# Optimization experiments

Hardware: AMD Instinct MI355X
Metric: run time of the kernel (lower is better)

Reference implementation:

```python
import jax, jax.numpy as jnp
from jax import lax
import numpy as np

B, CIN, COUT, T, H, W, KH, KW = 8, 256, 256, 16, 28, 28, 3, 3


def setup_inputs() -> dict:
    key = jax.random.key(0)
    k1, k2, k3 = jax.random.split(key, 3)
    x = jax.random.normal(k1, (B, CIN, T, H, W), dtype=jnp.float32)
    alpha = jax.random.uniform(k2, (B, CIN, T, 1, 1), dtype=jnp.float32)
    # base weight, kaiming-uniform-like init, stored as [1,1,c_out,c_in,kh,kw]
    fan_in = CIN * KH * KW
    bound = 1.0 / np.sqrt(fan_in)
    weight = jax.random.uniform(k3, (1, 1, COUT, CIN, KH, KW), dtype=jnp.float32,
                                minval=-bound, maxval=bound)
    return {"x": x, "alpha": alpha, "weight": weight}


def reference(x, alpha, weight):
    # x: [b, c_in, t, h, w]; alpha: [b, c_in, t, 1, 1]; weight: [1,1,c_out,c_in,kh,kw]
    b, c_in, t, h, w = x.shape
    c_out = weight.shape[2]
    w_base = weight[0, 0]  # [c_out, c_in, kh, kw]
    # W_t = alpha_t * W_base scales only input channels (alpha broadcasts over c_out),
    # so (alpha*W) conv x == W conv (alpha*x): modulate input, then one shared conv.
    xm = x * alpha  # [b, c_in, t, h, w]
    xm = jnp.transpose(xm, (0, 2, 1, 3, 4)).reshape(b * t, c_in, h, w)
    y = lax.conv_general_dilated(
        xm, w_base,
        window_strides=(1, 1),
        padding=((1, 1), (1, 1)),
        dimension_numbers=("NCHW", "OIHW", "NCHW"),
    )  # [b*t, c_out, h, w]
    oh, ow = y.shape[-2], y.shape[-1]
    y = y.reshape(b, t, c_out, oh, ow)
    return jnp.transpose(y, (0, 2, 1, 3, 4))  # [b, c_out, t, h, w]
```

## Files before the change

kernel.cpp:

```cpp
#include <hip/hip_runtime.h>
#include <hip/hip_bf16.h>
#include <cstdint>

#define CIN   256
#define COUT  256
#define NB    8
#define NT    16
#define NH    28
#define NW    28
#define HP    30
#define WP    30

#define XM_ELEMS   ((size_t)NB * NT * HP * WP * CIN)
#define XM_BYTES   (XM_ELEMS * 2)

typedef __bf16 bf16x8 __attribute__((ext_vector_type(8)));
typedef float  f32x4  __attribute__((ext_vector_type(4)));

#define AS1 __attribute__((address_space(1)))
#define AS3 __attribute__((address_space(3)))

static __device__ __forceinline__ unsigned short f2bf(float f) {
    __hip_bfloat16 h = __float2bfloat16(f);
    return __builtin_bit_cast(unsigned short, h);
}

__global__ void modulate_kernel(const float* __restrict__ x,
                                const float* __restrict__ alpha,
                                unsigned short* __restrict__ xm) {
    const int ci = threadIdx.x;
    const int blk = blockIdx.x;
    const int hp = blk % 30;
    const int bt = blk / 30;
    unsigned short* row = xm + (size_t)(bt * 900 + hp * 30) * 256;
    if (hp == 0 || hp == 29) {
        #pragma unroll
        for (int wp = 0; wp < 30; ++wp) row[wp * 256 + ci] = 0;
        return;
    }
    const int t = bt & 15, b = bt >> 4;
    const int h = hp - 1;
    const float a = alpha[(b * CIN + ci) * NT + t];
    const float* xrow = x + ((size_t)((b * CIN + ci) * NT + t) * NH + h) * NW;
    row[ci] = 0;
    row[29 * 256 + ci] = 0;
    const float4* xv = (const float4*)xrow;
    #pragma unroll
    for (int q = 0; q < 7; ++q) {
        float4 v = xv[q];
        row[(q * 4 + 1) * 256 + ci] = f2bf(v.x * a);
        row[(q * 4 + 2) * 256 + ci] = f2bf(v.y * a);
        row[(q * 4 + 3) * 256 + ci] = f2bf(v.z * a);
        row[(q * 4 + 4) * 256 + ci] = f2bf(v.w * a);
    }
}

__global__ void repack_w_kernel(const float* __restrict__ w,
                                unsigned short* __restrict__ wB) {
    const int ci = threadIdx.x;
    const int tap = blockIdx.x >> 8;
    const int co  = blockIdx.x & 255;
    wB[((tap * 256 + co) * 256) + ci] = f2bf(w[(co * 256 + ci) * 9 + tap]);
}


#define BAR()    __builtin_amdgcn_s_barrier()
#define LGKM0()  asm volatile("s_waitcnt lgkmcnt(0)" ::: "memory")
#define VMW(N)   asm volatile("s_waitcnt vmcnt(" #N ")" ::: "memory")
#define SCHED0() __builtin_amdgcn_sched_barrier(0)
#define PRIO(x)  __builtin_amdgcn_s_setprio(x)

#define STAGE_F(P) do {                                                       \
    const int kh2 = (tap2 * 11) >> 5;                                         \
    const int kw2 = tap2 - 3 * kh2;                                           \
    const int aOff = tap2 * 65536 + cic2 * 32;                                \
    const int bOff = ((kh2 - 1) * 30 + (kw2 - 1)) * 256 + cic2 * 32;          \
    _Pragma("unroll") for (int c_ = 0; c_ < 2; ++c_)                          \
        __builtin_amdgcn_global_load_lds(                                     \
            (const AS1 void*)(aSrc + aOff + c_ * 32768),                      \
            (AS3 void*)(lds + (P)*32768 + (c_*128 + wave*16)*64 + lane*16),   \
            16, 0, 0);                                                        \
    _Pragma("unroll") for (int c_ = 0; c_ < 2; ++c_)                          \
        __builtin_amdgcn_global_load_lds(                                     \
            (const AS1 void*)(bL[c_] + bOff),                                 \
            (AS3 void*)(lds + (P)*32768 + 16384 + (c_*128 + wave*16)*64 + lane*16), \
            16, 0, 0);                                                        \
    if (++tap2 == 9) { tap2 = 0; ++cic2; }                                    \
} while (0)

#define READF(S, P) do {                                                      \
    _Pragma("unroll") for (int m_ = 0; m_ < 4; ++m_)                          \
        fa##S[m_] = *(const bf16x8*)(lds + (P)*32768 +                        \
            (wm*64 + m_*16 + l15)*64 + readSwz);                              \
    _Pragma("unroll") for (int f_ = 0; f_ < 7; ++f_)                          \
        fb##S[f_] = *(const bf16x8*)(lds + (P)*32768 + 16384 +                \
            (wn*112 + f_*16 + l15)*64 + readSwz);                             \
} while (0)

#define MFMA28(S) do {                                                        \
    _Pragma("unroll") for (int m_ = 0; m_ < 4; ++m_)                          \
    _Pragma("unroll") for (int f_ = 0; f_ < 7; ++f_)                          \
        acc[m_][f_] = __builtin_amdgcn_mfma_f32_16x16x32_bf16(                \
            fb##S[f_], fa##S[m_], acc[m_][f_], 0, 0, 0);                      \
} while (0)

#define BODY_S(CS, NS, NBUF, SBUF) do {                                       \
    VMW(4);                                                                   \
    SCHED0();                                                                 \
    BAR();                                                                    \
    READF(NS, NBUF);                                                          \
    STAGE_F(SBUF);                                                            \
    SCHED0();                                                                 \
    PRIO(1); MFMA28(CS); PRIO(0);                                             \
    LGKM0();                                                                  \
    SCHED0();                                                                 \
} while (0)

#define BODY_N(CS, NS, NBUF, VMN) do {                                        \
    VMW(VMN);                                                                 \
    SCHED0();                                                                 \
    BAR();                                                                    \
    READF(NS, NBUF);                                                          \
    SCHED0();                                                                 \
    PRIO(1); MFMA28(CS); PRIO(0);                                             \
    LGKM0();                                                                  \
    SCHED0();                                                                 \
} while (0)

__global__ __launch_bounds__(512, 2) void conv_gemm_kernel(
    const unsigned short* __restrict__ xm,
    const unsigned short* __restrict__ wB,
    float* __restrict__ out) {
    __shared__ __align__(1024) char lds[98304];

    const int tid  = threadIdx.x;
    const int wave = tid >> 6;
    const int lane = tid & 63;
    const int l15  = lane & 15;
    const int n0   = blockIdx.x * 224;
    const int wm   = wave >> 1;
    const int wn   = wave & 1;

    const int swzE = 8 * ((lane & 3) ^ ((lane >> 3) & 3));
    const unsigned short* aSrc = wB + (wave * 16 + (lane >> 2)) * 256 + swzE;

    const unsigned short* bL[2];
    #pragma unroll
    for (int c_ = 0; c_ < 2; ++c_) {
        int nl = c_ * 128 + wave * 16 + (lane >> 2);
        nl = nl > 223 ? 223 : nl;
        const int n  = n0 + nl;
        const int w_ = n % 28, h_ = (n / 28) % 28, bt = n / 784;
        bL[c_] = xm + (size_t)((bt * 30 + h_ + 1) * 30 + (w_ + 1)) * 256 + swzE;
    }

    const int readSwz = ((lane >> 4) ^ ((l15 >> 1) & 3)) << 4;

    f32x4 acc[4][7];
    #pragma unroll
    for (int i = 0; i < 4; ++i)
        #pragma unroll
        for (int j = 0; j < 7; ++j) acc[i][j] = f32x4{0.f, 0.f, 0.f, 0.f};

    bf16x8 faA[4], fbA[7], faB[4], fbB[7];

    int tap2 = 0, cic2 = 0;
    STAGE_F(0);
    STAGE_F(1);
    STAGE_F(2);
    VMW(8);
    SCHED0();
    BAR();
    READF(A, 0);
    LGKM0();
    SCHED0();

    #pragma unroll 1
    for (int it = 0; it < 11; ++it) {
        BODY_S(A, B, 1, 0);
        BODY_S(B, A, 2, 1);
        BODY_S(A, B, 0, 2);
        BODY_S(B, A, 1, 0);
        BODY_S(A, B, 2, 1);
        BODY_S(B, A, 0, 2);
    }
    BODY_S(A, B, 1, 0);
    BODY_S(B, A, 2, 1);
    BODY_S(A, B, 0, 2);
    BODY_N(B, A, 1, 4);
    BODY_N(A, B, 2, 0);
    PRIO(1); MFMA28(B); PRIO(0);

    #pragma unroll
    for (int f = 0; f < 7; ++f) {
        const int n  = n0 + wn * 112 + f * 16 + ((lane >> 4) << 2);
        const int bt = n / 784;
        const int hw = n - bt * 784;
        const int b = bt >> 4, t = bt & 15;
        float* obase = out + ((size_t)(b * 256) * 16 + t) * 784 + hw;
        #pragma unroll
        for (int m = 0; m < 4; ++m) {
            const int co = wm * 64 + m * 16 + l15;
            *(f32x4*)(obase + (size_t)co * 12544) = acc[m][f];
        }
    }
}

extern "C" void kernel_launch(void* const* d_in, const int* in_sizes, int n_in,
                              void* d_out, int out_size, void* d_ws, size_t ws_size,
                              hipStream_t stream) {
    const float* x      = (const float*)d_in[0];
    const float* alpha  = (const float*)d_in[1];
    const float* weight = (const float*)d_in[2];
    float* out = (float*)d_out;

    unsigned short* xm = (unsigned short*)d_ws;
    unsigned short* wB = (unsigned short*)((char*)d_ws + XM_BYTES);

    modulate_kernel<<<dim3(NB * NT * HP), dim3(256), 0, stream>>>(x, alpha, xm);
    repack_w_kernel<<<dim3(9 * 256), dim3(256), 0, stream>>>(weight, wB);
    conv_gemm_kernel<<<dim3(448), dim3(512), 0, stream>>>(xm, wB, out);
}
```

Measured before the change: 158.3 us.

## Load weight fragments directly from global into registers, halve LDS staging

The weight (A) operand is no longer staged through LDS with global_load_lds. Each wave now reads its own weight fragments straight from global memory into registers, one step ahead of use. Only the activation tiles stay in the triple-buffered LDS ring, which halves the shared-memory footprint and could let two blocks share a CU. The cost is redundant global/L2 traffic for weights across waves, and the wait counts are retuned to cover the added in-flight loads, so exposed latency is a risk.

```diff
diff --git a/kernel.cpp b/kernel.cpp
--- a/kernel.cpp
+++ b/kernel.cpp
@@ -70,30 +70,28 @@
 #define SCHED0() __builtin_amdgcn_sched_barrier(0)
 #define PRIO(x)  __builtin_amdgcn_s_setprio(x)
 
-#define STAGE_F(P) do {                                                       \
-    const int kh2 = (tap2 * 11) >> 5;                                         \
-    const int kw2 = tap2 - 3 * kh2;                                           \
-    const int aOff = tap2 * 65536 + cic2 * 32;                                \
-    const int bOff = ((kh2 - 1) * 30 + (kw2 - 1)) * 256 + cic2 * 32;          \
-    _Pragma("unroll") for (int c_ = 0; c_ < 2; ++c_)                          \
-        __builtin_amdgcn_global_load_lds(                                     \
-            (const AS1 void*)(aSrc + aOff + c_ * 32768),                      \
-            (AS3 void*)(lds + (P)*32768 + (c_*128 + wave*16)*64 + lane*16),   \
-            16, 0, 0);                                                        \
+#define STAGE_B(P) do {                                                       \
+    const int kh2 = (tapS * 11) >> 5;                                         \
+    const int kw2 = tapS - 3 * kh2;                                           \
+    const int bOff = ((kh2 - 1) * 30 + (kw2 - 1)) * 256 + cicS * 32;          \
     _Pragma("unroll") for (int c_ = 0; c_ < 2; ++c_)                          \
         __builtin_amdgcn_global_load_lds(                                     \
             (const AS1 void*)(bL[c_] + bOff),                                 \
-            (AS3 void*)(lds + (P)*32768 + 16384 + (c_*128 + wave*16)*64 + lane*16), \
+            (AS3 void*)(lds + (P)*16384 + (c_*128 + wave*16)*64 + lane*16),   \
             16, 0, 0);                                                        \
-    if (++tap2 == 9) { tap2 = 0; ++cic2; }                                    \
-} while (0)
-
-#define READF(S, P) do {                                                      \
+    if (++tapS == 9) { tapS = 0; ++cicS; }                                    \
+} while (0)
+
+#define LOADA(S) do {                                                         \
+    const unsigned short* ap_ = aRow + tapA * 65536 + cicA * 32;              \
     _Pragma("unroll") for (int m_ = 0; m_ < 4; ++m_)                          \
-        fa##S[m_] = *(const bf16x8*)(lds + (P)*32768 +                        \
-            (wm*64 + m_*16 + l15)*64 + readSwz);                              \
+        fa##S[m_] = *(const bf16x8*)(ap_ + m_ * 4096);                        \
+    if (++tapA == 9) { tapA = 0; ++cicA; }                                    \
+} while (0)
+
+#define READF_B(S, P) do {                                                    \
     _Pragma("unroll") for (int f_ = 0; f_ < 7; ++f_)                          \
-        fb##S[f_] = *(const bf16x8*)(lds + (P)*32768 + 16384 +                \
+        fb##S[f_] = *(const bf16x8*)(lds + (P)*16384 +                        \
             (wn*112 + f_*16 + l15)*64 + readSwz);                             \
 } while (0)
 
@@ -105,11 +103,12 @@
 } while (0)
 
 #define BODY_S(CS, NS, NBUF, SBUF) do {                                       \
-    VMW(4);                                                                   \
+    VMW(6);                                                                   \
     SCHED0();                                                                 \
     BAR();                                                                    \
-    READF(NS, NBUF);                                                          \
-    STAGE_F(SBUF);                                                            \
+    READF_B(NS, NBUF);                                                        \
+    LOADA(NS);                                                                \
+    STAGE_B(SBUF);                                                            \
     SCHED0();                                                                 \
     PRIO(1); MFMA28(CS); PRIO(0);                                             \
     LGKM0();                                                                  \
@@ -120,7 +119,8 @@
     VMW(VMN);                                                                 \
     SCHED0();                                                                 \
     BAR();                                                                    \
-    READF(NS, NBUF);                                                          \
+    READF_B(NS, NBUF);                                                        \
+    LOADA(NS);                                                                \
     SCHED0();                                                                 \
     PRIO(1); MFMA28(CS); PRIO(0);                                             \
     LGKM0();                                                                  \
@@ -131,7 +131,7 @@
     const unsigned short* __restrict__ xm,
     const unsigned short* __restrict__ wB,
     float* __restrict__ out) {
-    __shared__ __align__(1024) char lds[98304];
+    __shared__ __align__(1024) char lds[49152];
 
     const int tid  = threadIdx.x;
     const int wave = tid >> 6;
@@ -141,9 +141,10 @@
     const int wm   = wave >> 1;
     const int wn   = wave & 1;
 
+    const unsigned short* aRow =
+        wB + (wm * 64 + l15) * 256 + (lane >> 4) * 8;
+
     const int swzE = 8 * ((lane & 3) ^ ((lane >> 3) & 3));
-    const unsigned short* aSrc = wB + (wave * 16 + (lane >> 2)) * 256 + swzE;
-
     const unsigned short* bL[2];
     #pragma unroll
     for (int c_ = 0; c_ < 2; ++c_) {
@@ -164,14 +165,17 @@
 
     bf16x8 faA[4], fbA[7], faB[4], fbB[7];
 
-    int tap2 = 0, cic2 = 0;
-    STAGE_F(0);
-    STAGE_F(1);
-    STAGE_F(2);
+    int tapS = 0, cicS = 0;
+    int tapA = 0, cicA = 0;
+
+    STAGE_B(0);
+    STAGE_B(1);
+    LOADA(A);
+    STAGE_B(2);
     VMW(8);
     SCHED0();
     BAR();
-    READF(A, 0);
+    READF_B(A, 0);
     LGKM0();
     SCHED0();
 
@@ -187,8 +191,8 @@
     BODY_S(A, B, 1, 0);
     BODY_S(B, A, 2, 1);
     BODY_S(A, B, 0, 2);
-    BODY_N(B, A, 1, 4);
-    BODY_N(A, B, 2, 0);
+    BODY_N(B, A, 1, 6);
+    BODY_N(A, B, 2, 4);
     PRIO(1); MFMA28(B); PRIO(0);
 
     #pragma unroll
```

Result: slower. 244.2 us (+54.2%).

## Shrink conv GEMM block tile to 256x112 with four waves

Applied to the files above, without the earlier changes.

The GEMM tile changes from 256 output channels by 224 pixels with 8 waves to 256 by 112 with 4 waves. Each wave now owns a full 64-channel slice across the whole 112-pixel column. The grid doubles to 896 blocks, and LDS per block drops to 72KB across three stages. The aim is better load balance across CUs and more resident blocks, at the cost of weight tiles being reloaded twice as often, which lowers arithmetic intensity per block.

```diff
diff --git a/kernel.cpp b/kernel.cpp
--- a/kernel.cpp
+++ b/kernel.cpp
@@ -71,30 +71,30 @@
 #define PRIO(x)  __builtin_amdgcn_s_setprio(x)
 
 #define STAGE_F(P) do {                                                       \
-    const int kh2 = (tap2 * 11) >> 5;                                         \
-    const int kw2 = tap2 - 3 * kh2;                                           \
-    const int aOff = tap2 * 65536 + cic2 * 32;                                \
-    const int bOff = ((kh2 - 1) * 30 + (kw2 - 1)) * 256 + cic2 * 32;          \
-    _Pragma("unroll") for (int c_ = 0; c_ < 2; ++c_)                          \
+    const int kh2 = (tapS * 11) >> 5;                                         \
+    const int kw2 = tapS - 3 * kh2;                                           \
+    const int aOff = tapS * 65536 + cicS * 32;                                \
+    const int bOff = ((kh2 - 1) * 30 + (kw2 - 1)) * 256 + cicS * 32;          \
+    _Pragma("unroll") for (int c_ = 0; c_ < 4; ++c_)                          \
         __builtin_amdgcn_global_load_lds(                                     \
-            (const AS1 void*)(aSrc + aOff + c_ * 32768),                      \
-            (AS3 void*)(lds + (P)*32768 + (c_*128 + wave*16)*64 + lane*16),   \
+            (const AS1 void*)(aSrc + aOff + c_ * 16384),                      \
+            (AS3 void*)(lds + (P)*24576 + (c_*64 + wv*16)*64 + lane*16),      \
             16, 0, 0);                                                        \
     _Pragma("unroll") for (int c_ = 0; c_ < 2; ++c_)                          \
         __builtin_amdgcn_global_load_lds(                                     \
             (const AS1 void*)(bL[c_] + bOff),                                 \
-            (AS3 void*)(lds + (P)*32768 + 16384 + (c_*128 + wave*16)*64 + lane*16), \
+            (AS3 void*)(lds + (P)*24576 + 16384 + (c_*64 + wv*16)*64 + lane*16), \
             16, 0, 0);                                                        \
-    if (++tap2 == 9) { tap2 = 0; ++cic2; }                                    \
+    if (++tapS == 9) { tapS = 0; ++cicS; }                                    \
 } while (0)
 
 #define READF(S, P) do {                                                      \
     _Pragma("unroll") for (int m_ = 0; m_ < 4; ++m_)                          \
-        fa##S[m_] = *(const bf16x8*)(lds + (P)*32768 +                        \
-            (wm*64 + m_*16 + l15)*64 + readSwz);                              \
+        fa##S[m_] = *(const bf16x8*)(lds + (P)*24576 +                        \
+            (wv*64 + m_*16 + l15)*64 + readSwz);                              \
     _Pragma("unroll") for (int f_ = 0; f_ < 7; ++f_)                          \
-        fb##S[f_] = *(const bf16x8*)(lds + (P)*32768 + 16384 +                \
-            (wn*112 + f_*16 + l15)*64 + readSwz);                             \
+        fb##S[f_] = *(const bf16x8*)(lds + (P)*24576 + 16384 +                \
+            (f_*16 + l15)*64 + readSwz);                                      \
 } while (0)
 
 #define MFMA28(S) do {                                                        \
@@ -105,7 +105,7 @@
 } while (0)
 
 #define BODY_S(CS, NS, NBUF, SBUF) do {                                       \
-    VMW(4);                                                                   \
+    VMW(6);                                                                   \
     SCHED0();                                                                 \
     BAR();                                                                    \
     READF(NS, NBUF);                                                          \
@@ -127,28 +127,26 @@
     SCHED0();                                                                 \
 } while (0)
 
-__global__ __launch_bounds__(512, 2) void conv_gemm_kernel(
+__global__ __launch_bounds__(256, 2) void conv_gemm_kernel(
     const unsigned short* __restrict__ xm,
     const unsigned short* __restrict__ wB,
     float* __restrict__ out) {
-    __shared__ __align__(1024) char lds[98304];
+    __shared__ __align__(1024) char lds[73728];
 
     const int tid  = threadIdx.x;
-    const int wave = tid >> 6;
+    const int wv   = tid >> 6;
     const int lane = tid & 63;
     const int l15  = lane & 15;
-    const int n0   = blockIdx.x * 224;
-    const int wm   = wave >> 1;
-    const int wn   = wave & 1;
+    const int n0   = blockIdx.x * 112;
 
     const int swzE = 8 * ((lane & 3) ^ ((lane >> 3) & 3));
-    const unsigned short* aSrc = wB + (wave * 16 + (lane >> 2)) * 256 + swzE;
+    const unsigned short* aSrc = wB + (wv * 16 + (lane >> 2)) * 256 + swzE;
 
     const unsigned short* bL[2];
     #pragma unroll
     for (int c_ = 0; c_ < 2; ++c_) {
-        int nl = c_ * 128 + wave * 16 + (lane >> 2);
-        nl = nl > 223 ? 223 : nl;
+        int nl = c_ * 64 + wv * 16 + (lane >> 2);
+        nl = nl > 111 ? 111 : nl;
         const int n  = n0 + nl;
         const int w_ = n % 28, h_ = (n / 28) % 28, bt = n / 784;
         bL[c_] = xm + (size_t)((bt * 30 + h_ + 1) * 30 + (w_ + 1)) * 256 + swzE;
@@ -164,11 +162,11 @@
 
     bf16x8 faA[4], fbA[7], faB[4], fbB[7];
 
-    int tap2 = 0, cic2 = 0;
+    int tapS = 0, cicS = 0;
     STAGE_F(0);
     STAGE_F(1);
     STAGE_F(2);
-    VMW(8);
+    VMW(12);
     SCHED0();
     BAR();
     READF(A, 0);
@@ -187,20 +185,20 @@
     BODY_S(A, B, 1, 0);
     BODY_S(B, A, 2, 1);
     BODY_S(A, B, 0, 2);
-    BODY_N(B, A, 1, 4);
+    BODY_N(B, A, 1, 6);
     BODY_N(A, B, 2, 0);
     PRIO(1); MFMA28(B); PRIO(0);
 
     #pragma unroll
     for (int f = 0; f < 7; ++f) {
-        const int n  = n0 + wn * 112 + f * 16 + ((lane >> 4) << 2);
+        const int n  = n0 + f * 16 + ((lane >> 4) << 2);
         const int bt = n / 784;
         const int hw = n - bt * 784;
         const int b = bt >> 4, t = bt & 15;
         float* obase = out + ((size_t)(b * 256) * 16 + t) * 784 + hw;
         #pragma unroll
         for (int m = 0; m < 4; ++m) {
-            const int co = wm * 64 + m * 16 + l15;
+            const int co = wv * 64 + m * 16 + l15;
             *(f32x4*)(obase + (size_t)co * 12544) = acc[m][f];
         }
     }
@@ -219,5 +217,5 @@
 
     modulate_kernel<<<dim3(NB * NT * HP), dim3(256), 0, stream>>>(x, alpha, xm);
     repack_w_kernel<<<dim3(9 * 256), dim3(256), 0, stream>>>(weight, wB);
-    conv_gemm_kernel<<<dim3(448), dim3(512), 0, stream>>>(xm, wB, out);
-}
+    conv_gemm_kernel<<<dim3(896), dim3(256), 0, stream>>>(xm, wB, out);
+}
```

Result: slower. 178.1 us (+12.5%).
